# Kernel tuning notes

Hardware: AMD Instinct MI355X
Metric: run time of the kernel (lower is better)

## Reference

```python
import jax, jax.numpy as jnp
import numpy as np

B, N, D, H = 8, 1024, 512, 8
HD = D // H
SCALE = 1.0 / np.sqrt(HD).astype(np.float32)


def setup_inputs() -> dict:
    key = jax.random.key(0)
    ks = jax.random.split(key, 7)
    x = jax.random.normal(ks[0], (B, N, D), dtype=jnp.float32)
    U = jax.random.normal(ks[1], (N, N), dtype=jnp.float32)
    attn_mask = jax.random.uniform(ks[2], (B, 1, 1, N), dtype=jnp.float32)
    # learned params: qkv projection D->3D and output projection D->D (with bias)
    w_qkv = jax.random.normal(ks[3], (D, 3 * D), dtype=jnp.float32) / np.sqrt(D).astype(np.float32)
    b_qkv = jnp.zeros((3 * D,), dtype=jnp.float32)
    w_out = jax.random.normal(ks[4], (D, D), dtype=jnp.float32) / np.sqrt(D).astype(np.float32)
    b_out = jnp.zeros((D,), dtype=jnp.float32)
    return {"x": x, "U": U, "attn_mask": attn_mask,
            "w_qkv": w_qkv, "b_qkv": b_qkv, "w_out": w_out, "b_out": b_out}


def reference(x, U, attn_mask, w_qkv, b_qkv, w_out, b_out):
    # QKV projection (QuantIdentity layers are identity in math; key_value = x)
    qkv = x @ w_qkv + b_qkv                       # [B, N, 3D]
    q, k, v = jnp.split(qkv, 3, axis=-1)          # each [B, N, D]

    def split_heads(t):
        return t.reshape(B, N, H, HD).transpose(0, 2, 1, 3)  # [B, H, N, HD]

    qh, kh, vh = split_heads(q), split_heads(k), split_heads(v)
    scores = jnp.einsum('bhqd,bhkd->bhqk', qh, kh) * SCALE   # [B, H, N, N]
    scores = scores + U[None, None, :, :]                    # additive interaction bias
    scores = scores + attn_mask                              # [B,1,1,N] broadcast add
    attn = jax.nn.softmax(scores, axis=-1)
    ctx = jnp.einsum('bhqk,bhkd->bhqd', attn, vh)            # [B, H, N, HD]
    ctx = ctx.transpose(0, 2, 1, 3).reshape(B, N, D)         # merge heads
    out = ctx @ w_out + b_out                                # [B, N, D]
    return out
```

## Files before the change

kernel.cpp:

```cpp
#include <hip/hip_runtime.h>

#define DEV __device__ __forceinline__

typedef __attribute__((ext_vector_type(8))) __bf16 bf16x8;
typedef __attribute__((ext_vector_type(4))) __bf16 bf16x4;
typedef __attribute__((ext_vector_type(4))) float f32x4;
typedef __attribute__((ext_vector_type(4))) float float4v;

typedef __attribute__((address_space(1))) const void ga_void;
typedef __attribute__((address_space(3))) void la_void;

constexpr float ATT_SCALE = 0.125f;

DEV void gload16(const void* g, void* l) {
  __builtin_amdgcn_global_load_lds((ga_void*)g, (la_void*)l, 16, 0, 0);
}

DEV f32x4 mfma_bf16(bf16x8 a, bf16x8 b, f32x4 c) {
  return __builtin_amdgcn_mfma_f32_16x16x32_bf16(a, b, c, 0, 0, 0);
}

__global__ __launch_bounds__(256) void cast_x_kernel(
    const float* __restrict__ in, __bf16* __restrict__ out, int n4) {
  int i = blockIdx.x * blockDim.x + threadIdx.x;
  int stride = gridDim.x * blockDim.x;
  for (; i < n4; i += stride) {
    float4v v = ((const float4v*)in)[i];
    bf16x4 o;
    o[0] = (__bf16)v[0]; o[1] = (__bf16)v[1];
    o[2] = (__bf16)v[2]; o[3] = (__bf16)v[3];
    ((bf16x4*)out)[i] = o;
  }
}

__global__ __launch_bounds__(256) void transpose_cast_kernel(
    const float* __restrict__ in, __bf16* __restrict__ out, int K, int Nc) {
  __shared__ float tile[32][33];
  int bx = blockIdx.x * 32;
  int by = blockIdx.y * 32;
  int tx = threadIdx.x, ty = threadIdx.y;
#pragma unroll
  for (int i = ty; i < 32; i += 8)
    tile[i][tx] = in[(size_t)(by + i) * Nc + bx + tx];
  __syncthreads();
#pragma unroll
  for (int i = ty; i < 32; i += 8)
    out[(size_t)(bx + i) * K + by + tx] = (__bf16)tile[tx][i];
}

__global__ __launch_bounds__(256) void gemm_qkv_kernel(
    const __bf16* __restrict__ A, const __bf16* __restrict__ Bt,
    const float* __restrict__ bias,
    __bf16* __restrict__ Qo, __bf16* __restrict__ Ko, __bf16* __restrict__ Vto) {
  __shared__ __align__(16) __bf16 As[2][128 * 32];
  __shared__ __align__(16) __bf16 Bs[2][128 * 32];
  const int tid = threadIdx.x;
  const int lane = tid & 63;
  const int w = tid >> 6;
  const int lr = lane & 15, lg = lane >> 4;
  const int m0 = blockIdx.x * 128, n0 = blockIdx.y * 128;
  const int wr = w >> 1, wc = w & 1;

  f32x4 acc[4][4] = {};

  auto stage = [&](int buf, int kt) {
#pragma unroll
    for (int cc = 0; cc < 2; ++cc) {
      int c = w * 2 + cc;
      int row = c * 16 + (lane >> 2);
      int slot = (lane & 3) ^ ((row >> 1) & 3);
      gload16(A + (size_t)(m0 + row) * 512 + kt * 32 + slot * 8, &As[buf][c * 512]);
      gload16(Bt + (size_t)(n0 + row) * 512 + kt * 32 + slot * 8, &Bs[buf][c * 512]);
    }
  };

  stage(0, 0);
  __syncthreads();
  for (int kt = 0; kt < 16; ++kt) {
    int cur = kt & 1;
    if (kt < 15) stage(cur ^ 1, kt + 1);
    bf16x8 av[4], bv[4];
#pragma unroll
    for (int i = 0; i < 4; ++i) {
      int row = wr * 64 + i * 16 + lr;
      av[i] = *(const bf16x8*)&As[cur][row * 32 + ((lg ^ ((row >> 1) & 3)) * 8)];
    }
#pragma unroll
    for (int j = 0; j < 4; ++j) {
      int row = wc * 64 + j * 16 + lr;
      bv[j] = *(const bf16x8*)&Bs[cur][row * 32 + ((lg ^ ((row >> 1) & 3)) * 8)];
    }
#pragma unroll
    for (int i = 0; i < 4; ++i)
#pragma unroll
      for (int j = 0; j < 4; ++j)
        acc[i][j] = mfma_bf16(av[i], bv[j], acc[i][j]);
    __syncthreads();
  }

  const int sec = n0 >> 9;
#pragma unroll
  for (int j = 0; j < 4; ++j) {
    int n = n0 + wc * 64 + j * 16 + lr;
    float bsv = bias[n];
    int nn = n & 511;
    int h = nn >> 6, d = nn & 63;
#pragma unroll
    for (int i = 0; i < 4; ++i) {
#pragma unroll
      for (int r = 0; r < 4; ++r) {
        int m = m0 + wr * 64 + i * 16 + lg * 4 + r;
        int b = m >> 10, nr = m & 1023;
        float v = acc[i][j][r] + bsv;
        if (sec == 0)
          Qo[(((size_t)(b * 8 + h)) * 1024 + nr) * 64 + d] = (__bf16)v;
        else if (sec == 1)
          Ko[(((size_t)(b * 8 + h)) * 1024 + nr) * 64 + d] = (__bf16)v;
        else
          Vto[(((size_t)(b * 8 + h)) * 64 + d) * 1024 + nr] = (__bf16)v;
      }
    }
  }
}

__global__ __launch_bounds__(256) void gemm_out_kernel(
    const __bf16* __restrict__ A, const __bf16* __restrict__ Bt,
    const float* __restrict__ bias, float* __restrict__ out) {
  __shared__ __align__(16) __bf16 As[2][128 * 32];
  __shared__ __align__(16) __bf16 Bs[2][128 * 32];
  const int tid = threadIdx.x;
  const int lane = tid & 63;
  const int w = tid >> 6;
  const int lr = lane & 15, lg = lane >> 4;
  const int m0 = blockIdx.x * 128, n0 = blockIdx.y * 128;
  const int wr = w >> 1, wc = w & 1;

  f32x4 acc[4][4] = {};

  auto stage = [&](int buf, int kt) {
#pragma unroll
    for (int cc = 0; cc < 2; ++cc) {
      int c = w * 2 + cc;
      int row = c * 16 + (lane >> 2);
      int slot = (lane & 3) ^ ((row >> 1) & 3);
      gload16(A + (size_t)(m0 + row) * 512 + kt * 32 + slot * 8, &As[buf][c * 512]);
      gload16(Bt + (size_t)(n0 + row) * 512 + kt * 32 + slot * 8, &Bs[buf][c * 512]);
    }
  };

  stage(0, 0);
  __syncthreads();
  for (int kt = 0; kt < 16; ++kt) {
    int cur = kt & 1;
    if (kt < 15) stage(cur ^ 1, kt + 1);
    bf16x8 av[4], bv[4];
#pragma unroll
    for (int i = 0; i < 4; ++i) {
      int row = wr * 64 + i * 16 + lr;
      av[i] = *(const bf16x8*)&As[cur][row * 32 + ((lg ^ ((row >> 1) & 3)) * 8)];
    }
#pragma unroll
    for (int j = 0; j < 4; ++j) {
      int row = wc * 64 + j * 16 + lr;
      bv[j] = *(const bf16x8*)&Bs[cur][row * 32 + ((lg ^ ((row >> 1) & 3)) * 8)];
    }
#pragma unroll
    for (int i = 0; i < 4; ++i)
#pragma unroll
      for (int j = 0; j < 4; ++j)
        acc[i][j] = mfma_bf16(av[i], bv[j], acc[i][j]);
    __syncthreads();
  }

#pragma unroll
  for (int j = 0; j < 4; ++j) {
    int n = n0 + wc * 64 + j * 16 + lr;
    float bsv = bias[n];
#pragma unroll
    for (int i = 0; i < 4; ++i) {
#pragma unroll
      for (int r = 0; r < 4; ++r) {
        int m = m0 + wr * 64 + i * 16 + lg * 4 + r;
        out[(size_t)m * 512 + n] = acc[i][j][r] + bsv;
      }
    }
  }
}

__global__ __launch_bounds__(256) void attn_kernel(
    const __bf16* __restrict__ Qh, const __bf16* __restrict__ Kh,
    const __bf16* __restrict__ Vth, const float* __restrict__ U,
    const float* __restrict__ mask, __bf16* __restrict__ ctx) {
  __shared__ __align__(16) __bf16 Ks[64 * 64];
  __shared__ __align__(16) __bf16 Vs[64 * 64];
  __shared__ __align__(16) __bf16 Ps[4][16 * 64];
  const int tid = threadIdx.x;
  const int lane = tid & 63;
  const int w = tid >> 6;
  const int lr = lane & 15, lg = lane >> 4;
  const int bh = blockIdx.x, qb = blockIdx.y;
  const int b = bh >> 3, h = bh & 7;

  bf16x8 qf[2];
  {
    const __bf16* qp = Qh + ((size_t)bh * 1024 + qb * 64 + w * 16 + lr) * 64;
    qf[0] = *(const bf16x8*)(qp + lg * 8);
    qf[1] = *(const bf16x8*)(qp + 32 + lg * 8);
  }

  f32x4 acc_o[4] = {};
  float m_run[4], l_run[4];
#pragma unroll
  for (int r = 0; r < 4; ++r) { m_run[r] = -3e38f; l_run[r] = 0.f; }

  const int strow = tid >> 2;
  const int stslot = (tid & 3) * 2;

  for (int kb = 0; kb < 16; ++kb) {
    __syncthreads();
    {
      const __bf16* kg = Kh + ((size_t)bh * 1024 + kb * 64 + strow) * 64 + stslot * 8;
      bf16x8 k0 = *(const bf16x8*)kg;
      bf16x8 k1 = *(const bf16x8*)(kg + 8);
      const __bf16* vg = Vth + ((size_t)bh * 64 + strow) * 1024 + kb * 64 + stslot * 8;
      bf16x8 v0 = *(const bf16x8*)vg;
      bf16x8 v1 = *(const bf16x8*)(vg + 8);
      int rbase = strow * 64;
      int sw = strow & 7;
      *(bf16x8*)&Ks[rbase + ((stslot ^ sw) * 8)] = k0;
      *(bf16x8*)&Ks[rbase + (((stslot + 1) ^ sw) * 8)] = k1;
      *(bf16x8*)&Vs[rbase + ((stslot ^ sw) * 8)] = v0;
      *(bf16x8*)&Vs[rbase + (((stslot + 1) ^ sw) * 8)] = v1;
    }
    __syncthreads();

    f32x4 sv[4];
#pragma unroll
    for (int t = 0; t < 4; ++t) {
      int krow = t * 16 + lr;
      const __bf16* kp = &Ks[krow * 64];
      int sw = krow & 7;
      bf16x8 k0 = *(const bf16x8*)(kp + ((lg ^ sw) * 8));
      bf16x8 k1 = *(const bf16x8*)(kp + (((4 + lg) ^ sw) * 8));
      f32x4 z = {0.f, 0.f, 0.f, 0.f};
      z = mfma_bf16(qf[0], k0, z);
      z = mfma_bf16(qf[1], k1, z);
      sv[t] = z;
    }

    float sval[4][4];
    int kc0 = kb * 64;
#pragma unroll
    for (int t = 0; t < 4; ++t) {
      int kcol = kc0 + t * 16 + lr;
      float mk = mask[b * 1024 + kcol];
#pragma unroll
      for (int r = 0; r < 4; ++r) {
        int qrow = qb * 64 + w * 16 + lg * 4 + r;
        sval[t][r] = sv[t][r] * ATT_SCALE + U[(size_t)qrow * 1024 + kcol] + mk;
      }
    }

    float pval[4][4];
#pragma unroll
    for (int r = 0; r < 4; ++r) {
      float mx = fmaxf(fmaxf(sval[0][r], sval[1][r]), fmaxf(sval[2][r], sval[3][r]));
      mx = fmaxf(mx, __shfl_xor(mx, 1));
      mx = fmaxf(mx, __shfl_xor(mx, 2));
      mx = fmaxf(mx, __shfl_xor(mx, 4));
      mx = fmaxf(mx, __shfl_xor(mx, 8));
      float mnew = fmaxf(m_run[r], mx);
      float f = __expf(m_run[r] - mnew);
      float ps = 0.f;
#pragma unroll
      for (int t = 0; t < 4; ++t) {
        float p = __expf(sval[t][r] - mnew);
        pval[t][r] = p;
        ps += p;
      }
      ps += __shfl_xor(ps, 1);
      ps += __shfl_xor(ps, 2);
      ps += __shfl_xor(ps, 4);
      ps += __shfl_xor(ps, 8);
      l_run[r] = l_run[r] * f + ps;
      m_run[r] = mnew;
#pragma unroll
      for (int t = 0; t < 4; ++t) acc_o[t][r] *= f;
    }

    {
      __bf16* pw = &Ps[w][0];
#pragma unroll
      for (int t = 0; t < 4; ++t)
#pragma unroll
        for (int r = 0; r < 4; ++r) {
          int q = lg * 4 + r;
          int k = t * 16 + lr;
          pw[q * 64 + (k ^ ((q & 7) << 3))] = (__bf16)pval[t][r];
        }
    }
    __syncthreads();

    bf16x8 pa0, pa1;
    {
      const __bf16* pp = &Ps[w][lr * 64];
      int sw = lr & 7;
      pa0 = *(const bf16x8*)(pp + ((lg ^ sw) * 8));
      pa1 = *(const bf16x8*)(pp + (((4 + lg) ^ sw) * 8));
    }
#pragma unroll
    for (int t = 0; t < 4; ++t) {
      int vrow = t * 16 + lr;
      const __bf16* vp = &Vs[vrow * 64];
      int sw = vrow & 7;
      bf16x8 v0 = *(const bf16x8*)(vp + ((lg ^ sw) * 8));
      bf16x8 v1 = *(const bf16x8*)(vp + (((4 + lg) ^ sw) * 8));
      acc_o[t] = mfma_bf16(pa0, v0, acc_o[t]);
      acc_o[t] = mfma_bf16(pa1, v1, acc_o[t]);
    }
  }

  float inv[4];
#pragma unroll
  for (int r = 0; r < 4; ++r) inv[r] = 1.0f / l_run[r];
#pragma unroll
  for (int t = 0; t < 4; ++t)
#pragma unroll
    for (int r = 0; r < 4; ++r) {
      int qrow = qb * 64 + w * 16 + lg * 4 + r;
      int d = t * 16 + lr;
      ctx[((size_t)(b * 1024 + qrow)) * 512 + h * 64 + d] = (__bf16)(acc_o[t][r] * inv[r]);
    }
}

extern "C" void kernel_launch(void* const* d_in, const int* in_sizes, int n_in,
                              void* d_out, int out_size, void* d_ws, size_t ws_size,
                              hipStream_t stream) {
  (void)in_sizes; (void)n_in; (void)out_size; (void)ws_size;
  const float* x     = (const float*)d_in[0];
  const float* U     = (const float*)d_in[1];
  const float* mask  = (const float*)d_in[2];
  const float* w_qkv = (const float*)d_in[3];
  const float* b_qkv = (const float*)d_in[4];
  const float* w_out = (const float*)d_in[5];
  const float* b_out = (const float*)d_in[6];
  float* out = (float*)d_out;

  char* p = (char*)d_ws;
  __bf16* xb    = (__bf16*)p; p += (size_t)8192 * 512 * 2;
  __bf16* wqkvT = (__bf16*)p; p += (size_t)1536 * 512 * 2;
  __bf16* woutT = (__bf16*)p; p += (size_t)512 * 512 * 2;
  __bf16* Qh    = (__bf16*)p; p += (size_t)64 * 1024 * 64 * 2;
  __bf16* Kh    = (__bf16*)p; p += (size_t)64 * 1024 * 64 * 2;
  __bf16* Vth   = (__bf16*)p; p += (size_t)64 * 64 * 1024 * 2;
  __bf16* ctx   = (__bf16*)p; p += (size_t)8192 * 512 * 2;

  hipLaunchKernelGGL(cast_x_kernel, dim3(2048), dim3(256), 0, stream,
                     x, xb, 8192 * 512 / 4);
  hipLaunchKernelGGL(transpose_cast_kernel, dim3(48, 16), dim3(32, 8), 0, stream,
                     w_qkv, wqkvT, 512, 1536);
  hipLaunchKernelGGL(transpose_cast_kernel, dim3(16, 16), dim3(32, 8), 0, stream,
                     w_out, woutT, 512, 512);
  hipLaunchKernelGGL(gemm_qkv_kernel, dim3(64, 12), dim3(256), 0, stream,
                     xb, wqkvT, b_qkv, Qh, Kh, Vth);
  hipLaunchKernelGGL(attn_kernel, dim3(64, 16), dim3(256), 0, stream,
                     Qh, Kh, Vth, U, mask, ctx);
  hipLaunchKernelGGL(gemm_out_kernel, dim3(64, 4), dim3(256), 0, stream,
                     ctx, woutT, b_out, out);
}
```

Before: 111.7 us.

## Double-buffer K/V via async LDS loads, stage U through LDS, lazy softmax rescale

Rewrites the attention inner loop so the next K/V tile is prefetched into a second LDS buffer with global_load_lds and the next U tile is loaded into registers, both overlapping the current tile's compute. U is staged coalesced into LDS, and the same LDS region is reused for the P tile. Softmax switches to exp2 with log2e folded into the scale and mask, and the running-max rescale only happens when the max grows by more than 8 in log2 units. This cuts global-load latency stalls and per-row transcendental work. The cost is more LDS use and shared-buffer aliasing that depends on correct barrier placement.

```diff
diff --git a/kernel.cpp b/kernel.cpp
--- a/kernel.cpp
+++ b/kernel.cpp
@@ -10,7 +10,14 @@
 typedef __attribute__((address_space(1))) const void ga_void;
 typedef __attribute__((address_space(3))) void la_void;
 
-constexpr float ATT_SCALE = 0.125f;
+constexpr float LOG2E = 1.44269504089f;
+constexpr float ATT_SCALE2 = 0.125f * 1.44269504089f;
+
+#if __has_builtin(__builtin_amdgcn_exp2f)
+#define EXP2(x) __builtin_amdgcn_exp2f(x)
+#else
+#define EXP2(x) exp2f(x)
+#endif
 
 DEV void gload16(const void* g, void* l) {
   __builtin_amdgcn_global_load_lds((ga_void*)g, (la_void*)l, 16, 0, 0);
@@ -191,9 +198,9 @@
     const __bf16* __restrict__ Qh, const __bf16* __restrict__ Kh,
     const __bf16* __restrict__ Vth, const float* __restrict__ U,
     const float* __restrict__ mask, __bf16* __restrict__ ctx) {
-  __shared__ __align__(16) __bf16 Ks[64 * 64];
-  __shared__ __align__(16) __bf16 Vs[64 * 64];
-  __shared__ __align__(16) __bf16 Ps[4][16 * 64];
+  __shared__ __align__(16) __bf16 Ks[2][64 * 64];
+  __shared__ __align__(16) __bf16 Vs[2][64 * 64];
+  __shared__ __align__(16) float Us[64 * 68];
   const int tid = threadIdx.x;
   const int lane = tid & 63;
   const int w = tid >> 6;
@@ -213,32 +220,58 @@
 #pragma unroll
   for (int r = 0; r < 4; ++r) { m_run[r] = -3e38f; l_run[r] = 0.f; }
 
-  const int strow = tid >> 2;
-  const int stslot = (tid & 3) * 2;
+  auto stageKV = [&](int buf, int kb) {
+#pragma unroll
+    for (int i = 0; i < 2; ++i) {
+      int gid = i * 256 + tid;
+      int row = gid >> 3, slot = gid & 7;
+      int sg = slot ^ (row & 7);
+      gload16(Kh + ((size_t)bh * 1024 + kb * 64 + row) * 64 + sg * 8,
+              &Ks[buf][(i * 256 + w * 64) * 8]);
+      gload16(Vth + ((size_t)bh * 64 + row) * 1024 + kb * 64 + sg * 8,
+              &Vs[buf][(i * 256 + w * 64) * 8]);
+    }
+  };
+
+  const int urow = lane >> 2, uc4 = lane & 3;
+  float4v ur[4];
+  auto loadU = [&](int kb) {
+    const float* up = U + (size_t)(qb * 64 + w * 16 + urow) * 1024 + kb * 64 + uc4 * 4;
+#pragma unroll
+    for (int j = 0; j < 4; ++j) ur[j] = *(const float4v*)(up + 16 * j);
+  };
+  auto writeU = [&]() {
+    float* dst = &Us[(w * 16 + urow) * 68 + uc4 * 4];
+#pragma unroll
+    for (int j = 0; j < 4; ++j) *(float4v*)(dst + 16 * j) = ur[j];
+  };
+
+  __bf16* pw = (__bf16*)&Us[(size_t)w * 16 * 68];
+
+  stageKV(0, 0);
+  loadU(0);
+  float mk2[4];
+#pragma unroll
+  for (int t = 0; t < 4; ++t) mk2[t] = mask[b * 1024 + t * 16 + lr] * LOG2E;
+  writeU();
+  __syncthreads();
 
   for (int kb = 0; kb < 16; ++kb) {
-    __syncthreads();
-    {
-      const __bf16* kg = Kh + ((size_t)bh * 1024 + kb * 64 + strow) * 64 + stslot * 8;
-      bf16x8 k0 = *(const bf16x8*)kg;
-      bf16x8 k1 = *(const bf16x8*)(kg + 8);
-      const __bf16* vg = Vth + ((size_t)bh * 64 + strow) * 1024 + kb * 64 + stslot * 8;
-      bf16x8 v0 = *(const bf16x8*)vg;
-      bf16x8 v1 = *(const bf16x8*)(vg + 8);
-      int rbase = strow * 64;
-      int sw = strow & 7;
-      *(bf16x8*)&Ks[rbase + ((stslot ^ sw) * 8)] = k0;
-      *(bf16x8*)&Ks[rbase + (((stslot + 1) ^ sw) * 8)] = k1;
-      *(bf16x8*)&Vs[rbase + ((stslot ^ sw) * 8)] = v0;
-      *(bf16x8*)&Vs[rbase + (((stslot + 1) ^ sw) * 8)] = v1;
-    }
-    __syncthreads();
+    const int cur = kb & 1;
+    float mkraw[4];
+    if (kb < 15) {
+      stageKV(cur ^ 1, kb + 1);
+      loadU(kb + 1);
+#pragma unroll
+      for (int t = 0; t < 4; ++t)
+        mkraw[t] = mask[b * 1024 + (kb + 1) * 64 + t * 16 + lr];
+    }
 
     f32x4 sv[4];
 #pragma unroll
     for (int t = 0; t < 4; ++t) {
       int krow = t * 16 + lr;
-      const __bf16* kp = &Ks[krow * 64];
+      const __bf16* kp = &Ks[cur][krow * 64];
       int sw = krow & 7;
       bf16x8 k0 = *(const bf16x8*)(kp + ((lg ^ sw) * 8));
       bf16x8 k1 = *(const bf16x8*)(kp + (((4 + lg) ^ sw) * 8));
@@ -249,32 +282,45 @@
     }
 
     float sval[4][4];
-    int kc0 = kb * 64;
 #pragma unroll
     for (int t = 0; t < 4; ++t) {
-      int kcol = kc0 + t * 16 + lr;
-      float mk = mask[b * 1024 + kcol];
 #pragma unroll
       for (int r = 0; r < 4; ++r) {
-        int qrow = qb * 64 + w * 16 + lg * 4 + r;
-        sval[t][r] = sv[t][r] * ATT_SCALE + U[(size_t)qrow * 1024 + kcol] + mk;
-      }
-    }
-
+        float uv = Us[(w * 16 + lg * 4 + r) * 68 + t * 16 + lr];
+        sval[t][r] = fmaf(uv, LOG2E, fmaf(sv[t][r], ATT_SCALE2, mk2[t]));
+      }
+    }
+
+    float mx[4];
+#pragma unroll
+    for (int r = 0; r < 4; ++r) {
+      float m = fmaxf(fmaxf(sval[0][r], sval[1][r]), fmaxf(sval[2][r], sval[3][r]));
+      m = fmaxf(m, __shfl_xor(m, 1));
+      m = fmaxf(m, __shfl_xor(m, 2));
+      m = fmaxf(m, __shfl_xor(m, 4));
+      m = fmaxf(m, __shfl_xor(m, 8));
+      mx[r] = m;
+    }
+    bool grow = (mx[0] > m_run[0] + 8.f) || (mx[1] > m_run[1] + 8.f) ||
+                (mx[2] > m_run[2] + 8.f) || (mx[3] > m_run[3] + 8.f);
+    if (__any(grow)) {
+#pragma unroll
+      for (int r = 0; r < 4; ++r) {
+        float mnew = fmaxf(m_run[r], mx[r]);
+        float f = EXP2(m_run[r] - mnew);
+        m_run[r] = mnew;
+        l_run[r] *= f;
+#pragma unroll
+        for (int t = 0; t < 4; ++t) acc_o[t][r] *= f;
+      }
+    }
     float pval[4][4];
 #pragma unroll
     for (int r = 0; r < 4; ++r) {
-      float mx = fmaxf(fmaxf(sval[0][r], sval[1][r]), fmaxf(sval[2][r], sval[3][r]));
-      mx = fmaxf(mx, __shfl_xor(mx, 1));
-      mx = fmaxf(mx, __shfl_xor(mx, 2));
-      mx = fmaxf(mx, __shfl_xor(mx, 4));
-      mx = fmaxf(mx, __shfl_xor(mx, 8));
-      float mnew = fmaxf(m_run[r], mx);
-      float f = __expf(m_run[r] - mnew);
       float ps = 0.f;
 #pragma unroll
       for (int t = 0; t < 4; ++t) {
-        float p = __expf(sval[t][r] - mnew);
+        float p = EXP2(sval[t][r] - m_run[r]);
         pval[t][r] = p;
         ps += p;
       }
@@ -282,28 +328,21 @@
       ps += __shfl_xor(ps, 2);
       ps += __shfl_xor(ps, 4);
       ps += __shfl_xor(ps, 8);
-      l_run[r] = l_run[r] * f + ps;
-      m_run[r] = mnew;
-#pragma unroll
-      for (int t = 0; t < 4; ++t) acc_o[t][r] *= f;
-    }
-
-    {
-      __bf16* pw = &Ps[w][0];
-#pragma unroll
-      for (int t = 0; t < 4; ++t)
-#pragma unroll
-        for (int r = 0; r < 4; ++r) {
-          int q = lg * 4 + r;
-          int k = t * 16 + lr;
-          pw[q * 64 + (k ^ ((q & 7) << 3))] = (__bf16)pval[t][r];
-        }
-    }
-    __syncthreads();
+      l_run[r] += ps;
+    }
+
+#pragma unroll
+    for (int t = 0; t < 4; ++t)
+#pragma unroll
+      for (int r = 0; r < 4; ++r) {
+        int q = lg * 4 + r;
+        int k = t * 16 + lr;
+        pw[q * 64 + (k ^ ((q & 7) << 3))] = (__bf16)pval[t][r];
+      }
 
     bf16x8 pa0, pa1;
     {
-      const __bf16* pp = &Ps[w][lr * 64];
+      const __bf16* pp = &pw[lr * 64];
       int sw = lr & 7;
       pa0 = *(const bf16x8*)(pp + ((lg ^ sw) * 8));
       pa1 = *(const bf16x8*)(pp + (((4 + lg) ^ sw) * 8));
@@ -311,13 +350,20 @@
 #pragma unroll
     for (int t = 0; t < 4; ++t) {
       int vrow = t * 16 + lr;
-      const __bf16* vp = &Vs[vrow * 64];
+      const __bf16* vp = &Vs[cur][vrow * 64];
       int sw = vrow & 7;
       bf16x8 v0 = *(const bf16x8*)(vp + ((lg ^ sw) * 8));
       bf16x8 v1 = *(const bf16x8*)(vp + (((4 + lg) ^ sw) * 8));
       acc_o[t] = mfma_bf16(pa0, v0, acc_o[t]);
       acc_o[t] = mfma_bf16(pa1, v1, acc_o[t]);
     }
+
+    if (kb < 15) {
+      writeU();
+#pragma unroll
+      for (int t = 0; t < 4; ++t) mk2[t] = mkraw[t] * LOG2E;
+    }
+    __syncthreads();
   }
 
   float inv[4];
```

After: 123.8 us. 1.11x slower.
